# Performance work log

Hardware: AMD Instinct MI355X
Metric: run time of the kernel (lower is better)

## Reference

```python
import jax, jax.numpy as jnp
import numpy as np

NU, NBU, NI, D, L = 50000, 20000, 100000, 64, 2
C_TEMP = 0.25


def setup_inputs() -> dict:
    key = jax.random.key(0)
    ks = jax.random.split(key, 11)
    B, E_ui, E_ub, E_bi = 2048, 1_500_000, 1_000_000, 1_000_000
    return {
        "users": jax.random.randint(ks[0], (B,), 0, NU, dtype=jnp.int32),
        "bundles": jax.random.randint(ks[1], (B, 2), 0, NBU, dtype=jnp.int32),
        "ui_u": jax.random.randint(ks[2], (E_ui,), 0, NU, dtype=jnp.int32),
        "ui_i": jax.random.randint(ks[3], (E_ui,), 0, NI, dtype=jnp.int32),
        "ub_u": jax.random.randint(ks[4], (E_ub,), 0, NU, dtype=jnp.int32),
        "ub_b": jax.random.randint(ks[5], (E_ub,), 0, NBU, dtype=jnp.int32),
        "bi_b": jax.random.randint(ks[6], (E_bi,), 0, NBU, dtype=jnp.int32),
        "bi_i": jax.random.randint(ks[7], (E_bi,), 0, NI, dtype=jnp.int32),
        "users_feature": jax.random.normal(ks[8], (NU, D), jnp.float32) * 0.1,
        "bundles_feature": jax.random.normal(ks[9], (NBU, D), jnp.float32) * 0.1,
        "items_feature": jax.random.normal(ks[10], (NI, D), jnp.float32) * 0.1,
    }


def _sym_norm_vals(rows, cols, n):
    # laplace_transform: D_r^{-1/2} A D_c^{-1/2}; graph is symmetric so row/col degrees coincide
    deg = jax.ops.segment_sum(jnp.ones(rows.shape, jnp.float32), rows, num_segments=n)
    dinv = 1.0 / (jnp.sqrt(deg) + 1e-8)
    return dinv[rows] * dinv[cols]


def _spmm(rows, cols, vals, feat, n):
    return jax.ops.segment_sum(vals[:, None] * feat[cols], rows, num_segments=n)


def _one_propagate(rows, cols, n, A, Bf):
    vals = _sym_norm_vals(rows, cols, n)
    f = jnp.concatenate([A, Bf], axis=0)  # [n, D]
    acc = f
    for i in range(L):
        f = _spmm(rows, cols, vals, f, n) / (i + 2)
        nrm = jnp.maximum(jnp.linalg.norm(f, axis=1, keepdims=True), 1e-12)
        acc = acc + f / nrm  # sum of L2-normalized layer outputs + layer0
    return acc[: A.shape[0]], acc[A.shape[0]:]


def _bundle_agg(bi_b, bi_i, il_items):
    # row-normalized bundle-item aggregation: diag(1/bundle_size) @ BI
    deg = jax.ops.segment_sum(jnp.ones(bi_b.shape, jnp.float32), bi_b, num_segments=NBU)
    w = (1.0 / (deg + 1e-8))[bi_b]
    return jax.ops.segment_sum(w[:, None] * il_items[bi_i], bi_b, num_segments=NBU)


def _c_loss(pos, aug):
    pos = pos[:, 0, :]
    aug = aug[:, 0, :]
    pos = pos / jnp.maximum(jnp.linalg.norm(pos, axis=1, keepdims=True), 1e-12)
    aug = aug / jnp.maximum(jnp.linalg.norm(aug, axis=1, keepdims=True), 1e-12)
    pos_score = jnp.sum(pos * aug, axis=1) / C_TEMP
    ttl = jnp.matmul(pos, aug.T) / C_TEMP  # [B, B]
    return -jnp.mean(pos_score - jax.nn.logsumexp(ttl, axis=1))


def reference(users, bundles, ui_u, ui_i, ub_u, ub_b, bi_b, bi_i,
              users_feature, bundles_feature, items_feature):
    # item-level graph: [[0, UI], [UI^T, 0]], size NU+NI (symmetric directed edge list)
    il_rows = jnp.concatenate([ui_u, ui_i + NU])
    il_cols = jnp.concatenate([ui_i + NU, ui_u])
    IL_users, IL_items = _one_propagate(il_rows, il_cols, NU + NI, users_feature, items_feature)
    IL_bundles = _bundle_agg(bi_b, bi_i, IL_items)

    # bundle-level graph: [[0, UB], [UB^T, 0]], size NU+NBU
    bl_rows = jnp.concatenate([ub_u, ub_b + NU])
    bl_cols = jnp.concatenate([ub_b + NU, ub_u])
    BL_users, BL_bundles = _one_propagate(bl_rows, bl_cols, NU + NBU, users_feature, bundles_feature)

    nb = bundles.shape[1]
    IL_u = jnp.broadcast_to(IL_users[users][:, None, :], (users.shape[0], nb, D))
    BL_u = jnp.broadcast_to(BL_users[users][:, None, :], (users.shape[0], nb, D))
    IL_b = IL_bundles[bundles]  # [B, nb, D]
    BL_b = BL_bundles[bundles]

    pred = jnp.sum(IL_u * IL_b, axis=2) + jnp.sum(BL_u * BL_b, axis=2)  # [B, 2]
    bpr_loss = -jnp.mean(jax.nn.log_sigmoid(pred[:, 0:1] - pred[:, 1:2]))

    c_loss = 0.5 * (_c_loss(IL_u, BL_u) + _c_loss(IL_b, BL_b))
    return jnp.stack([bpr_loss, c_loss])


if __name__ == "__main__":
    out = reference(**setup_inputs())
    print(out)
```

## Files before the change

kernel.cpp:

```cpp
#include <hip/hip_runtime.h>
#include <hip/hip_bf16.h>
#include <math.h>

static constexpr int NUc  = 50000;
static constexpr int NBUc = 20000;
static constexpr int NIc  = 100000;
static constexpr int NILc = 150000;
static constexpr int NBLc = 70000;
static constexpr int GUB0   = 150016;
static constexpr int GBI0   = 220032;
static constexpr int BK_UB0 = 1172;
static constexpr int BK_BI0 = 1719;
static constexpr int NBK    = 1876;
static constexpr int GTOT   = NBK * 128;

__device__ __forceinline__ float wredsum(float v) {
  #pragma unroll
  for (int m = 32; m >= 1; m >>= 1) v += __shfl_xor(v, m, 64);
  return v;
}
__device__ __forceinline__ float bf2f(unsigned short h) {
  return __uint_as_float(((unsigned int)h) << 16);
}
__device__ __forceinline__ unsigned short f2bf(float f) {
  unsigned int u = __float_as_uint(f);
  return (unsigned short)((u + 0x7FFFu + ((u >> 16) & 1u)) >> 16);
}

__global__ void k_bcount_all(const int* __restrict__ ui_u, const int* __restrict__ ui_i,
                             const int* __restrict__ ub_u, const int* __restrict__ ub_b,
                             const int* __restrict__ bi_b,
                             int E_ui, int E_ub, int E_bi, int* __restrict__ bCnt) {
  __shared__ int hist[NBK];
  for (int i = threadIdx.x; i < NBK; i += 256) hist[i] = 0;
  __syncthreads();
  int b = blockIdx.x;
  if (b < 512) {
    int chunk = (E_ui + 511) / 512, c0 = b * chunk, c1 = min(E_ui, c0 + chunk);
    for (int e = c0 + (int)threadIdx.x; e < c1; e += 256) {
      atomicAdd(&hist[ui_u[e] >> 7], 1);
      atomicAdd(&hist[(ui_i[e] + NUc) >> 7], 1);
    }
  } else if (b < 768) {
    int lb = b - 512, chunk = (E_ub + 255) / 256, c0 = lb * chunk, c1 = min(E_ub, c0 + chunk);
    for (int e = c0 + (int)threadIdx.x; e < c1; e += 256) {
      atomicAdd(&hist[(GUB0 + ub_u[e]) >> 7], 1);
      atomicAdd(&hist[(GUB0 + NUc + ub_b[e]) >> 7], 1);
    }
  } else {
    int lb = b - 768, chunk = (E_bi + 255) / 256, c0 = lb * chunk, c1 = min(E_bi, c0 + chunk);
    for (int e = c0 + (int)threadIdx.x; e < c1; e += 256)
      atomicAdd(&hist[(GBI0 + bi_b[e]) >> 7], 1);
  }
  __syncthreads();
  for (int i = threadIdx.x; i < NBK; i += 256)
    if (hist[i]) atomicAdd(&bCnt[i], hist[i]);
}

__global__ void k_scan2048(const int* __restrict__ in, int n,
                           int* __restrict__ outBase, int* __restrict__ outCur) {
  __shared__ int sh[512];
  int t = threadIdx.x, i0 = 4 * t;
  int v0 = (i0 < n) ? in[i0] : 0;
  int v1 = (i0 + 1 < n) ? in[i0 + 1] : 0;
  int v2 = (i0 + 2 < n) ? in[i0 + 2] : 0;
  int v3 = (i0 + 3 < n) ? in[i0 + 3] : 0;
  int ts = v0 + v1 + v2 + v3;
  sh[t] = ts;
  __syncthreads();
  for (int o = 1; o < 512; o <<= 1) {
    int x = (t >= o) ? sh[t - o] : 0;
    __syncthreads();
    sh[t] += x;
    __syncthreads();
  }
  int ex = sh[t] - ts;
  if (i0 < n)     { outBase[i0] = ex;                    outCur[i0] = ex; }
  if (i0 + 1 < n) { outBase[i0 + 1] = ex + v0;           outCur[i0 + 1] = ex + v0; }
  if (i0 + 2 < n) { outBase[i0 + 2] = ex + v0 + v1;      outCur[i0 + 2] = ex + v0 + v1; }
  if (i0 + 3 < n) { outBase[i0 + 3] = ex + v0 + v1 + v2; outCur[i0 + 3] = ex + v0 + v1 + v2; }
  if (t == 511) outBase[n] = sh[511];
}

__global__ void k_bin_all(const int* __restrict__ ui_u, const int* __restrict__ ui_i,
                          const int* __restrict__ ub_u, const int* __restrict__ ub_b,
                          const int* __restrict__ bi_b, const int* __restrict__ bi_i,
                          int E_ui, int E_ub, int E_bi,
                          int* __restrict__ bCur, int2* __restrict__ binned) {
  __shared__ int hist[NBK];
  __shared__ int base[NBK];
  for (int i = threadIdx.x; i < NBK; i += 256) hist[i] = 0;
  __syncthreads();
  int b = blockIdx.x;
  int c0, c1, seg;
  if (b < 512)      { seg = 0; int ch = (E_ui + 511) / 512; c0 = b * ch; c1 = min(E_ui, c0 + ch); }
  else if (b < 768) { seg = 1; int ch = (E_ub + 255) / 256; c0 = (b - 512) * ch; c1 = min(E_ub, c0 + ch); }
  else              { seg = 2; int ch = (E_bi + 255) / 256; c0 = (b - 768) * ch; c1 = min(E_bi, c0 + ch); }
  for (int e = c0 + (int)threadIdx.x; e < c1; e += 256) {
    if (seg == 0) {
      atomicAdd(&hist[ui_u[e] >> 7], 1);
      atomicAdd(&hist[(ui_i[e] + NUc) >> 7], 1);
    } else if (seg == 1) {
      atomicAdd(&hist[(GUB0 + ub_u[e]) >> 7], 1);
      atomicAdd(&hist[(GUB0 + NUc + ub_b[e]) >> 7], 1);
    } else {
      atomicAdd(&hist[(GBI0 + bi_b[e]) >> 7], 1);
    }
  }
  __syncthreads();
  for (int i = threadIdx.x; i < NBK; i += 256) {
    int h = hist[i];
    base[i] = h ? atomicAdd(&bCur[i], h) : 0;
    hist[i] = 0;
  }
  __syncthreads();
  for (int e = c0 + (int)threadIdx.x; e < c1; e += 256) {
    if (seg == 0) {
      int u = ui_u[e], x = ui_i[e] + NUc;
      int b1 = u >> 7; binned[base[b1] + atomicAdd(&hist[b1], 1)] = make_int2(u, x);
      int b2 = x >> 7; binned[base[b2] + atomicAdd(&hist[b2], 1)] = make_int2(x, u);
    } else if (seg == 1) {
      int ul = ub_u[e], bl = NUc + ub_b[e];
      int r1 = GUB0 + ul, r2 = GUB0 + bl;
      int b1 = r1 >> 7; binned[base[b1] + atomicAdd(&hist[b1], 1)] = make_int2(r1, bl);
      int b2 = r2 >> 7; binned[base[b2] + atomicAdd(&hist[b2], 1)] = make_int2(r2, ul);
    } else {
      int r = GBI0 + bi_b[e];
      int b1 = r >> 7; binned[base[b1] + atomicAdd(&hist[b1], 1)] = make_int2(r, bi_i[e]);
    }
  }
}

__global__ void k_rowhist_all(const int2* __restrict__ binned, const int* __restrict__ bBase,
                              int* __restrict__ cnt) {
  __shared__ int hist[128];
  int bk = blockIdx.x, rowbase = bk << 7;
  int s = bBase[bk], e = bBase[bk + 1];
  if (threadIdx.x < 128) hist[threadIdx.x] = 0;
  __syncthreads();
  for (int i = s + (int)threadIdx.x; i < e; i += 256)
    atomicAdd(&hist[binned[i].x & 127], 1);
  __syncthreads();
  if (threadIdx.x < 128) cnt[rowbase + (int)threadIdx.x] = hist[threadIdx.x];
}

__global__ void k_scan_block_pad(const int* __restrict__ in, int n, int* __restrict__ out,
                                 int* __restrict__ bsum) {
  __shared__ int sh[256];
  int t = threadIdx.x;
  long base = (long)blockIdx.x * 1024 + (long)t * 4;
  int v0 = (base     < n) ? ((in[base]     + 15) & ~15) : 0;
  int v1 = (base + 1 < n) ? ((in[base + 1] + 15) & ~15) : 0;
  int v2 = (base + 2 < n) ? ((in[base + 2] + 15) & ~15) : 0;
  int v3 = (base + 3 < n) ? ((in[base + 3] + 15) & ~15) : 0;
  int tsum = v0 + v1 + v2 + v3;
  sh[t] = tsum;
  __syncthreads();
  for (int o = 1; o < 256; o <<= 1) {
    int x = (t >= o) ? sh[t - o] : 0;
    __syncthreads();
    sh[t] += x;
    __syncthreads();
  }
  int excl = sh[t] - tsum;
  if (t == 255) bsum[blockIdx.x] = sh[255];
  if (base     < n) out[base]     = excl;
  if (base + 1 < n) out[base + 1] = excl + v0;
  if (base + 2 < n) out[base + 2] = excl + v0 + v1;
  if (base + 3 < n) out[base + 3] = excl + v0 + v1 + v2;
}

__global__ void k_scan_bsum(int* __restrict__ bsum, int nb) {
  __shared__ int sh[256];
  int t = threadIdx.x;
  int v = (t < nb) ? bsum[t] : 0;
  sh[t] = v;
  __syncthreads();
  for (int o = 1; o < 256; o <<= 1) {
    int x = (t >= o) ? sh[t - o] : 0;
    __syncthreads();
    sh[t] += x;
    __syncthreads();
  }
  if (t < nb) bsum[t] = sh[t] - v;
}

__global__ void k_scan_add(int* __restrict__ out, int n, const int* __restrict__ bsum) {
  long i = (long)blockIdx.x * 256 + threadIdx.x;
  if (i < n) out[i] += bsum[i >> 10];
}

__global__ void k_csrfill_all(const int2* __restrict__ binned, const int* __restrict__ bBase,
                              const int* __restrict__ rp, int* __restrict__ colv) {
  __shared__ int cur[128];
  int bk = blockIdx.x, rowbase = bk << 7;
  int xb, zpad;
  if (bk < BK_UB0)      { xb = 0;    zpad = NILc; }
  else if (bk < BK_BI0) { xb = GUB0; zpad = GUB0 + NBLc; }
  else                  { xb = 0;    zpad = NIc; }
  int s = bBase[bk], e = bBase[bk + 1];
  if (threadIdx.x < 128) cur[threadIdx.x] = rp[rowbase + (int)threadIdx.x];
  __syncthreads();
  for (int i = s + (int)threadIdx.x; i < e; i += 256) {
    int2 rc = binned[i];
    int pos = atomicAdd(&cur[rc.x & 127], 1);
    colv[pos] = xb + rc.y;
  }
  __syncthreads();
  if (threadIdx.x < 128) {
    int r = rowbase + (int)threadIdx.x;
    int end = rp[r + 1];
    for (int k = cur[threadIdx.x]; k < end; k++) colv[k] = zpad;
  }
}

__global__ void k_prescale_all(const int* __restrict__ cnt, const float* __restrict__ userF,
                               const float* __restrict__ bundF, const float* __restrict__ itemF,
                               unsigned short* __restrict__ X) {
  long idx = (long)blockIdx.x * 256 + threadIdx.x;
  if (idx >= (long)GBI0 * 64) return;
  int g = (int)(idx >> 6), d = (int)(idx & 63);
  float v = 0.0f;
  if (g < NILc) v = (g < NUc) ? userF[(long)g * 64 + d] : itemF[(long)(g - NUc) * 64 + d];
  else if (g >= GUB0 && g < GUB0 + NBLc) {
    int l = g - GUB0;
    v = (l < NUc) ? userF[(long)l * 64 + d] : bundF[(long)(l - NUc) * 64 + d];
  }
  float dinv = 1.0f / (sqrtf((float)cnt[g]) + 1e-8f);
  X[idx] = f2bf(v * dinv);
}

__global__ void k_spmm_g(const int* __restrict__ rp, const int* __restrict__ cnt,
                         const int* __restrict__ col, const unsigned short* __restrict__ X,
                         unsigned short* __restrict__ outB, float* __restrict__ outInv,
                         float scale, int mulDinv, int n) {
  int row = blockIdx.x * 4 + (threadIdx.x >> 6);
  if (row >= n) return;
  int lane = threadIdx.x & 63, q = lane >> 4, p = lane & 15;
  int s = rp[row], e = rp[row + 1];
  const uint2* Xp = (const uint2*)X + p;
  float a0 = 0.f, a1 = 0.f, a2 = 0.f, a3 = 0.f;
  for (int eo = s + q; eo < e; eo += 16) {
    int c0 = col[eo], c1 = col[eo + 4], c2 = col[eo + 8], c3 = col[eo + 12];
    uint2 v0 = Xp[(size_t)c0 << 4];
    uint2 v1 = Xp[(size_t)c1 << 4];
    uint2 v2 = Xp[(size_t)c2 << 4];
    uint2 v3 = Xp[(size_t)c3 << 4];
    a0 += (__uint_as_float(v0.x << 16) + __uint_as_float(v1.x << 16)) +
          (__uint_as_float(v2.x << 16) + __uint_as_float(v3.x << 16));
    a1 += (__uint_as_float(v0.x & 0xFFFF0000u) + __uint_as_float(v1.x & 0xFFFF0000u)) +
          (__uint_as_float(v2.x & 0xFFFF0000u) + __uint_as_float(v3.x & 0xFFFF0000u));
    a2 += (__uint_as_float(v0.y << 16) + __uint_as_float(v1.y << 16)) +
          (__uint_as_float(v2.y << 16) + __uint_as_float(v3.y << 16));
    a3 += (__uint_as_float(v0.y & 0xFFFF0000u) + __uint_as_float(v1.y & 0xFFFF0000u)) +
          (__uint_as_float(v2.y & 0xFFFF0000u) + __uint_as_float(v3.y & 0xFFFF0000u));
  }
  a0 += __shfl_xor(a0, 32, 64); a1 += __shfl_xor(a1, 32, 64);
  a2 += __shfl_xor(a2, 32, 64); a3 += __shfl_xor(a3, 32, 64);
  a0 += __shfl_xor(a0, 16, 64); a1 += __shfl_xor(a1, 16, 64);
  a2 += __shfl_xor(a2, 16, 64); a3 += __shfl_xor(a3, 16, 64);
  float dinv = 1.0f / (sqrtf((float)cnt[row]) + 1e-8f);
  float f = dinv * scale;
  float r0 = a0 * f, r1 = a1 * f, r2 = a2 * f, r3 = a3 * f;
  float ss = r0 * r0 + r1 * r1 + r2 * r2 + r3 * r3;
  ss += __shfl_xor(ss, 8, 64); ss += __shfl_xor(ss, 4, 64);
  ss += __shfl_xor(ss, 2, 64); ss += __shfl_xor(ss, 1, 64);
  if (q == 0) {
    float mf = mulDinv ? dinv : 1.0f;
    uint2 m;
    m.x = (unsigned int)f2bf(r0 * mf) | ((unsigned int)f2bf(r1 * mf) << 16);
    m.y = (unsigned int)f2bf(r2 * mf) | ((unsigned int)f2bf(r3 * mf) << 16);
    *(uint2*)(outB + (size_t)row * 64 + p * 4) = m;
    if (p == 0) outInv[row] = 1.0f / fmaxf(sqrtf(ss), 1e-12f);
  }
}

__global__ void k_agg_g(const int* __restrict__ rp, const int* __restrict__ cnt,
                        const int* __restrict__ col, const unsigned short* __restrict__ MACC,
                        float* __restrict__ ILB, int n) {
  int rl = blockIdx.x * 4 + (threadIdx.x >> 6);
  if (rl >= n) return;
  int row = GBI0 + rl;
  int lane = threadIdx.x & 63, q = lane >> 4, p = lane & 15;
  int s = rp[row], e = rp[row + 1];
  const uint2* Xp = (const uint2*)MACC + p;
  float a0 = 0.f, a1 = 0.f, a2 = 0.f, a3 = 0.f;
  for (int eo = s + q; eo < e; eo += 16) {
    int c0 = col[eo], c1 = col[eo + 4], c2 = col[eo + 8], c3 = col[eo + 12];
    uint2 v0 = Xp[(size_t)c0 << 4];
    uint2 v1 = Xp[(size_t)c1 << 4];
    uint2 v2 = Xp[(size_t)c2 << 4];
    uint2 v3 = Xp[(size_t)c3 << 4];
    a0 += (__uint_as_float(v0.x << 16) + __uint_as_float(v1.x << 16)) +
          (__uint_as_float(v2.x << 16) + __uint_as_float(v3.x << 16));
    a1 += (__uint_as_float(v0.x & 0xFFFF0000u) + __uint_as_float(v1.x & 0xFFFF0000u)) +
          (__uint_as_float(v2.x & 0xFFFF0000u) + __uint_as_float(v3.x & 0xFFFF0000u));
    a2 += (__uint_as_float(v0.y << 16) + __uint_as_float(v1.y << 16)) +
          (__uint_as_float(v2.y << 16) + __uint_as_float(v3.y << 16));
    a3 += (__uint_as_float(v0.y & 0xFFFF0000u) + __uint_as_float(v1.y & 0xFFFF0000u)) +
          (__uint_as_float(v2.y & 0xFFFF0000u) + __uint_as_float(v3.y & 0xFFFF0000u));
  }
  a0 += __shfl_xor(a0, 32, 64); a1 += __shfl_xor(a1, 32, 64);
  a2 += __shfl_xor(a2, 32, 64); a3 += __shfl_xor(a3, 32, 64);
  a0 += __shfl_xor(a0, 16, 64); a1 += __shfl_xor(a1, 16, 64);
  a2 += __shfl_xor(a2, 16, 64); a3 += __shfl_xor(a3, 16, 64);
  if (q == 0) {
    float w = 1.0f / ((float)cnt[row] + 1e-8f);
    *(float4*)(ILB + (size_t)rl * 64 + p * 4) = make_float4(a0 * w, a1 * w, a2 * w, a3 * w);
  }
}

__global__ void k_acc_all(const float* __restrict__ userF, const float* __restrict__ bundF,
                          const float* __restrict__ itemF, const int* __restrict__ cnt,
                          const unsigned short* __restrict__ M1, const unsigned short* __restrict__ F2b,
                          const float* __restrict__ INV1, const float* __restrict__ INV2,
                          float* __restrict__ ACC, unsigned short* __restrict__ MACC) {
  long idx = (long)blockIdx.x * 256 + threadIdx.x;
  if (idx >= (long)(NILc + NBLc) * 64) return;
  int rl = (int)(idx >> 6), d = (int)(idx & 63);
  int g; float base;
  bool il = rl < NILc;
  if (il) {
    g = rl;
    base = (rl < NUc) ? userF[(long)rl * 64 + d] : itemF[(long)(rl - NUc) * 64 + d];
  } else {
    int l = rl - NILc;
    g = GUB0 + l;
    base = (l < NUc) ? userF[(long)l * 64 + d] : bundF[(long)(l - NUc) * 64 + d];
  }
  float rs = sqrtf((float)cnt[g]) + 1e-8f;
  float F1 = bf2f(M1[(size_t)g * 64 + d]) * rs;
  float F2 = bf2f(F2b[(size_t)g * 64 + d]);
  float res = base + F1 * INV1[g] + F2 * INV2[g];
  ACC[idx] = res;
  if (il && rl >= NUc) MACC[(size_t)(rl - NUc) * 64 + d] = f2bf(res);
}

__global__ void k_gather_all(const int* __restrict__ users, const int* __restrict__ bundles,
                             const float* __restrict__ ACC, const float* __restrict__ ILB, int B,
                             float* __restrict__ ILu, float* __restrict__ BLu,
                             float* __restrict__ ILb2, float* __restrict__ BLb2) {
  long i = (long)blockIdx.x * 256 + threadIdx.x;
  if (i >= (long)6 * B * 64) return;
  int r = (int)(i >> 6), d = (int)(i & 63);
  if (r < B) ILu[(long)r * 64 + d] = ACC[(long)users[r] * 64 + d];
  else if (r < 2 * B) { int rr = r - B; BLu[(long)rr * 64 + d] = ACC[(long)(NILc + users[rr]) * 64 + d]; }
  else if (r < 4 * B) { int rr = r - 2 * B; ILb2[(long)rr * 64 + d] = ILB[(long)bundles[rr] * 64 + d]; }
  else { int rr = r - 4 * B; BLb2[(long)rr * 64 + d] = ACC[(long)(NILc + NUc + bundles[rr]) * 64 + d]; }
}

__global__ void k_normalize4(const float* __restrict__ s0, const float* __restrict__ s1,
                             const float* __restrict__ s2, const float* __restrict__ s3,
                             float* __restrict__ d0, float* __restrict__ d1,
                             float* __restrict__ d2, float* __restrict__ d3, int B) {
  int row = blockIdx.x * 4 + (threadIdx.x >> 6);
  int lane = threadIdx.x & 63;
  if (row >= 4 * B) return;
  int which = row / B, r = row - which * B;
  const float* src; float* dst; int stride;
  if (which == 0)      { src = s0; dst = d0; stride = 64; }
  else if (which == 1) { src = s1; dst = d1; stride = 64; }
  else if (which == 2) { src = s2; dst = d2; stride = 128; }
  else                 { src = s3; dst = d3; stride = 128; }
  float v = src[(long)r * stride + lane];
  float ss = wredsum(v * v);
  dst[(long)r * 64 + lane] = v * (1.0f / fmaxf(sqrtf(ss), 1e-12f));
}

__global__ void k_bpr(const float* __restrict__ ILu, const float* __restrict__ ILb2,
                      const float* __restrict__ BLu, const float* __restrict__ BLb2,
                      int B, float* __restrict__ out) {
  int row = blockIdx.x * 4 + (threadIdx.x >> 6);
  int lane = threadIdx.x & 63;
  if (row >= B) return;
  float t = ILu[(long)row * 64 + lane] *
              (ILb2[(long)(2 * row) * 64 + lane] - ILb2[(long)(2 * row + 1) * 64 + lane]) +
            BLu[(long)row * 64 + lane] *
              (BLb2[(long)(2 * row) * 64 + lane] - BLb2[(long)(2 * row + 1) * 64 + lane]);
  float x = wredsum(t);
  if (lane == 0) {
    float ls = -(fmaxf(-x, 0.0f) + log1pf(expf(-fabsf(x))));
    unsafeAtomicAdd(&out[0], -ls / (float)B);
  }
}

__global__ void k_gemm_nt2(const float* __restrict__ P1, const float* __restrict__ A1,
                           const float* __restrict__ P2, const float* __restrict__ A2,
                           float* __restrict__ S1o, float* __restrict__ S2o,
                           int N, float scale) {
  __shared__ float Ps[64][129];
  __shared__ float As[64][129];
  const float* P = blockIdx.z ? P2 : P1;
  const float* A = blockIdx.z ? A2 : A1;
  float* S = blockIdx.z ? S2o : S1o;
  int bi0 = blockIdx.y * 128, bj0 = blockIdx.x * 128;
  int t = threadIdx.x;
  #pragma unroll
  for (int sct = 0; sct < 8; sct++) {
    int idx4 = t + sct * 256;
    int r = idx4 >> 4, k = (idx4 & 15) << 2;
    int pr = min(bi0 + r, N - 1);
    int ar = min(bj0 + r, N - 1);
    float4 v = *(const float4*)(P + (long)pr * 64 + k);
    Ps[k][r] = v.x; Ps[k + 1][r] = v.y; Ps[k + 2][r] = v.z; Ps[k + 3][r] = v.w;
    float4 w = *(const float4*)(A + (long)ar * 64 + k);
    As[k][r] = w.x; As[k + 1][r] = w.y; As[k + 2][r] = w.z; As[k + 3][r] = w.w;
  }
  __syncthreads();
  int tx = t & 15, ty = t >> 4;
  float acc[8][8];
  #pragma unroll
  for (int i = 0; i < 8; i++)
    #pragma unroll
    for (int j = 0; j < 8; j++) acc[i][j] = 0.0f;
  #pragma unroll 4
  for (int k = 0; k < 64; k++) {
    float a[8], b[8];
    #pragma unroll
    for (int i = 0; i < 8; i++) a[i] = Ps[k][ty * 8 + i];
    #pragma unroll
    for (int j = 0; j < 8; j++) b[j] = As[k][tx + 16 * j];
    #pragma unroll
    for (int i = 0; i < 8; i++)
      #pragma unroll
      for (int j = 0; j < 8; j++) acc[i][j] = fmaf(a[i], b[j], acc[i][j]);
  }
  #pragma unroll
  for (int i = 0; i < 8; i++) {
    int row = bi0 + ty * 8 + i;
    if (row >= N) continue;
    #pragma unroll
    for (int j = 0; j < 8; j++) {
      int cc = bj0 + tx + 16 * j;
      if (cc < N) S[(long)row * N + cc] = acc[i][j] * scale;
    }
  }
}

__global__ void k_lse2(const float* __restrict__ S1, const float* __restrict__ S2,
                       int B, float coeff, float* __restrict__ out) {
  constexpr float L2E = 1.44269504f;
  int row = blockIdx.x * 4 + (threadIdx.x >> 6);
  int lane = threadIdx.x & 63;
  const float* Sr; int dg;
  if (row < B) { Sr = S1 + (long)row * B; dg = row; }
  else         { Sr = S2 + (long)(row - B) * B; dg = row - B; }
  float m = -1e30f, s = 0.0f;
  for (int w = 0; w < (B >> 8); w++) {
    float4 v = *(const float4*)(Sr + ((w << 6) + lane) * 4);
    float mx = fmaxf(fmaxf(v.x, v.y), fmaxf(v.z, v.w));
    if (mx > m) { s *= exp2f((m - mx) * L2E); m = mx; }
    s += exp2f((v.x - m) * L2E) + exp2f((v.y - m) * L2E) +
         exp2f((v.z - m) * L2E) + exp2f((v.w - m) * L2E);
  }
  #pragma unroll
  for (int o = 32; o >= 1; o >>= 1) {
    float m2 = __shfl_xor(m, o, 64), s2 = __shfl_xor(s, o, 64);
    float M = fmaxf(m, m2);
    s = s * exp2f((m - M) * L2E) + s2 * exp2f((m2 - M) * L2E);
    m = M;
  }
  if (lane == 0) {
    float lse = m + log2f(s) * 0.69314718f;
    unsafeAtomicAdd(&out[1], -(Sr[dg] - lse) * coeff);
  }
}

extern "C" void kernel_launch(void* const* d_in, const int* in_sizes, int n_in,
                              void* d_out, int out_size, void* d_ws, size_t ws_size,
                              hipStream_t stream) {
  const int* users   = (const int*)d_in[0];
  const int* bundles = (const int*)d_in[1];
  const int* ui_u    = (const int*)d_in[2];
  const int* ui_i    = (const int*)d_in[3];
  const int* ub_u    = (const int*)d_in[4];
  const int* ub_b    = (const int*)d_in[5];
  const int* bi_b    = (const int*)d_in[6];
  const int* bi_i    = (const int*)d_in[7];
  const float* userF = (const float*)d_in[8];
  const float* bundF = (const float*)d_in[9];
  const float* itemF = (const float*)d_in[10];
  float* out = (float*)d_out;

  const int B    = in_sizes[0];
  const int E_ui = in_sizes[2];
  const int E_ub = in_sizes[4];
  const int E_bi = in_sizes[6];
  const long E_all = 2L * E_ui + 2L * E_ub + E_bi;

  float* ws = (float*)d_ws;
  size_t off = 0;
  auto alloc = [&](size_t nfloat) -> float* {
    float* p = ws + off;
    off += (nfloat + 63) & ~(size_t)63;
    return p;
  };
  float* ACC = alloc((size_t)(NILc + NBLc) * 64);
  unsigned short* X  = (unsigned short*)alloc((size_t)GBI0 * 32);
  unsigned short* M1 = (unsigned short*)alloc((size_t)GBI0 * 32);
  int2* binned = (int2*)alloc((size_t)E_all * 2);
  int* colv  = (int*)alloc((size_t)E_all + 15 * (size_t)GTOT + 128);
  int* rp    = (int*)alloc(GTOT + 1);
  int* cnt   = (int*)alloc(GTOT + 1);
  float* INV1 = alloc(GTOT);
  float* INV2 = alloc(GTOT);
  float* ILB  = alloc((size_t)NBUc * 64);
  float* ILu  = alloc((size_t)B * 64);
  float* BLu  = alloc((size_t)B * 64);
  float* ILb2 = alloc((size_t)B * 128);
  float* BLb2 = alloc((size_t)B * 128);
  float* PN1  = alloc((size_t)B * 64);
  float* AN1  = alloc((size_t)B * 64);
  float* PN2  = alloc((size_t)B * 64);
  float* AN2  = alloc((size_t)B * 64);
  int* bCnt  = (int*)alloc(2049);
  int* bBase = (int*)alloc(2049);
  int* bCur  = (int*)alloc(2049);
  int* bsum  = (int*)alloc(256);
  (void)ws_size; (void)n_in; (void)out_size;

  unsigned short* F2b  = X;
  unsigned short* MACC = (unsigned short*)binned;
  float* S1 = ACC;
  float* S2 = ACC + (size_t)B * B;

  hipMemsetAsync(bCnt, 0, sizeof(int) * NBK, stream);
  k_bcount_all<<<1024, 256, 0, stream>>>(ui_u, ui_i, ub_u, ub_b, bi_b, E_ui, E_ub, E_bi, bCnt);
  k_scan2048<<<1, 512, 0, stream>>>(bCnt, NBK, bBase, bCur);
  k_bin_all<<<1024, 256, 0, stream>>>(ui_u, ui_i, ub_u, ub_b, bi_b, bi_i,
                                      E_ui, E_ub, E_bi, bCur, binned);
  hipMemsetAsync(cnt, 0, sizeof(int) * (GTOT + 1), stream);
  k_rowhist_all<<<NBK, 256, 0, stream>>>(binned, bBase, cnt);
  {
    int scan_n = GTOT + 1;
    int nb1 = (scan_n + 1023) / 1024;
    k_scan_block_pad<<<nb1, 256, 0, stream>>>(cnt, scan_n, rp, bsum);
    k_scan_bsum<<<1, 256, 0, stream>>>(bsum, nb1);
    k_scan_add<<<(scan_n + 255) / 256, 256, 0, stream>>>(rp, scan_n, bsum);
  }
  k_csrfill_all<<<NBK, 256, 0, stream>>>(binned, bBase, rp, colv);

  k_prescale_all<<<(int)(((long)GBI0 * 64 + 255) / 256), 256, 0, stream>>>(cnt, userF, bundF,
                                                                           itemF, X);
  k_spmm_g<<<(GBI0 + 3) / 4, 256, 0, stream>>>(rp, cnt, colv, X, M1, INV1, 0.5f, 1, GBI0);
  k_spmm_g<<<(GBI0 + 3) / 4, 256, 0, stream>>>(rp, cnt, colv, M1, F2b, INV2, 1.0f / 3.0f, 0, GBI0);
  hipMemsetAsync(MACC + (size_t)NIc * 64, 0, 128, stream);
  k_acc_all<<<(int)(((long)(NILc + NBLc) * 64 + 255) / 256), 256, 0, stream>>>(
      userF, bundF, itemF, cnt, M1, F2b, INV1, INV2, ACC, MACC);
  k_agg_g<<<(NBUc + 3) / 4, 256, 0, stream>>>(rp, cnt, colv, MACC, ILB, NBUc);
  k_gather_all<<<(int)(((long)6 * B * 64 + 255) / 256), 256, 0, stream>>>(
      users, bundles, ACC, ILB, B, ILu, BLu, ILb2, BLb2);

  hipMemsetAsync(out, 0, 2 * sizeof(float), stream);
  k_bpr<<<(B + 3) / 4, 256, 0, stream>>>(ILu, ILb2, BLu, BLb2, B, out);
  k_normalize4<<<(4 * B + 3) / 4, 256, 0, stream>>>(ILu, BLu, ILb2, BLb2, PN1, AN1, PN2, AN2, B);
  dim3 gg((B + 127) / 128, (B + 127) / 128, 2);
  k_gemm_nt2<<<gg, 256, 0, stream>>>(PN1, AN1, PN2, AN2, S1, S2, B, 4.0f);
  k_lse2<<<(2 * B + 3) / 4, 256, 0, stream>>>(S1, S2, B, 0.5f / (float)B, out);
}
```

Baseline: 575.7 us.

## Pack binned edges into 32 bits and compute accumulations only for batch rows

Edge records in the binning stage are packed into one 32-bit word: the row's low 7 bits sit in the top bits and the column in the low 18 bits. This halves the scatter and read traffic of the intermediate edge buffer. The full-size ACC accumulation over all user, bundle and item rows is replaced by an items-only pass feeding bundle aggregation, plus a per-batch kernel that computes user and bundle accumulations on demand. That kernel also does the L2 normalization, removing the separate gather and normalize kernels and the large ACC buffer. The similarity matrices now reuse the X and M1 buffers, which relies on column indices staying below 2^18 and on those buffers being dead by the GEMM.

```diff
diff --git a/kernel.cpp b/kernel.cpp
--- a/kernel.cpp
+++ b/kernel.cpp
@@ -86,7 +86,7 @@
                           const int* __restrict__ ub_u, const int* __restrict__ ub_b,
                           const int* __restrict__ bi_b, const int* __restrict__ bi_i,
                           int E_ui, int E_ub, int E_bi,
-                          int* __restrict__ bCur, int2* __restrict__ binned) {
+                          int* __restrict__ bCur, unsigned int* __restrict__ binned) {
   __shared__ int hist[NBK];
   __shared__ int base[NBK];
   for (int i = threadIdx.x; i < NBK; i += 256) hist[i] = 0;
@@ -117,21 +117,26 @@
   for (int e = c0 + (int)threadIdx.x; e < c1; e += 256) {
     if (seg == 0) {
       int u = ui_u[e], x = ui_i[e] + NUc;
-      int b1 = u >> 7; binned[base[b1] + atomicAdd(&hist[b1], 1)] = make_int2(u, x);
-      int b2 = x >> 7; binned[base[b2] + atomicAdd(&hist[b2], 1)] = make_int2(x, u);
+      int b1 = u >> 7;
+      binned[base[b1] + atomicAdd(&hist[b1], 1)] = ((unsigned)(u & 127) << 18) | (unsigned)x;
+      int b2 = x >> 7;
+      binned[base[b2] + atomicAdd(&hist[b2], 1)] = ((unsigned)(x & 127) << 18) | (unsigned)u;
     } else if (seg == 1) {
       int ul = ub_u[e], bl = NUc + ub_b[e];
       int r1 = GUB0 + ul, r2 = GUB0 + bl;
-      int b1 = r1 >> 7; binned[base[b1] + atomicAdd(&hist[b1], 1)] = make_int2(r1, bl);
-      int b2 = r2 >> 7; binned[base[b2] + atomicAdd(&hist[b2], 1)] = make_int2(r2, ul);
+      int b1 = r1 >> 7;
+      binned[base[b1] + atomicAdd(&hist[b1], 1)] = ((unsigned)(r1 & 127) << 18) | (unsigned)bl;
+      int b2 = r2 >> 7;
+      binned[base[b2] + atomicAdd(&hist[b2], 1)] = ((unsigned)(r2 & 127) << 18) | (unsigned)ul;
     } else {
       int r = GBI0 + bi_b[e];
-      int b1 = r >> 7; binned[base[b1] + atomicAdd(&hist[b1], 1)] = make_int2(r, bi_i[e]);
+      int b1 = r >> 7;
+      binned[base[b1] + atomicAdd(&hist[b1], 1)] = ((unsigned)(r & 127) << 18) | (unsigned)bi_i[e];
     }
   }
 }
 
-__global__ void k_rowhist_all(const int2* __restrict__ binned, const int* __restrict__ bBase,
+__global__ void k_rowhist_all(const unsigned int* __restrict__ binned, const int* __restrict__ bBase,
                               int* __restrict__ cnt) {
   __shared__ int hist[128];
   int bk = blockIdx.x, rowbase = bk << 7;
@@ -139,7 +144,7 @@
   if (threadIdx.x < 128) hist[threadIdx.x] = 0;
   __syncthreads();
   for (int i = s + (int)threadIdx.x; i < e; i += 256)
-    atomicAdd(&hist[binned[i].x & 127], 1);
+    atomicAdd(&hist[binned[i] >> 18], 1);
   __syncthreads();
   if (threadIdx.x < 128) cnt[rowbase + (int)threadIdx.x] = hist[threadIdx.x];
 }
@@ -190,7 +195,7 @@
   if (i < n) out[i] += bsum[i >> 10];
 }
 
-__global__ void k_csrfill_all(const int2* __restrict__ binned, const int* __restrict__ bBase,
+__global__ void k_csrfill_all(const unsigned int* __restrict__ binned, const int* __restrict__ bBase,
                               const int* __restrict__ rp, int* __restrict__ colv) {
   __shared__ int cur[128];
   int bk = blockIdx.x, rowbase = bk << 7;
@@ -202,9 +207,9 @@
   if (threadIdx.x < 128) cur[threadIdx.x] = rp[rowbase + (int)threadIdx.x];
   __syncthreads();
   for (int i = s + (int)threadIdx.x; i < e; i += 256) {
-    int2 rc = binned[i];
-    int pos = atomicAdd(&cur[rc.x & 127], 1);
-    colv[pos] = xb + rc.y;
+    unsigned int pk = binned[i];
+    int pos = atomicAdd(&cur[pk >> 18], 1);
+    colv[pos] = xb + (int)(pk & 0x3FFFFu);
   }
   __syncthreads();
   if (threadIdx.x < 128) {
@@ -310,61 +315,64 @@
   }
 }
 
-__global__ void k_acc_all(const float* __restrict__ userF, const float* __restrict__ bundF,
-                          const float* __restrict__ itemF, const int* __restrict__ cnt,
-                          const unsigned short* __restrict__ M1, const unsigned short* __restrict__ F2b,
-                          const float* __restrict__ INV1, const float* __restrict__ INV2,
-                          float* __restrict__ ACC, unsigned short* __restrict__ MACC) {
+__global__ void k_acc_items(const float* __restrict__ itemF, const int* __restrict__ cnt,
+                            const unsigned short* __restrict__ M1, const unsigned short* __restrict__ F2b,
+                            const float* __restrict__ INV1, const float* __restrict__ INV2,
+                            unsigned short* __restrict__ MACC) {
   long idx = (long)blockIdx.x * 256 + threadIdx.x;
-  if (idx >= (long)(NILc + NBLc) * 64) return;
-  int rl = (int)(idx >> 6), d = (int)(idx & 63);
-  int g; float base;
-  bool il = rl < NILc;
-  if (il) {
-    g = rl;
-    base = (rl < NUc) ? userF[(long)rl * 64 + d] : itemF[(long)(rl - NUc) * 64 + d];
+  if (idx >= (long)NIc * 64) return;
+  int rl = (int)(idx >> 6);
+  int g = NUc + rl;
+  long gi = (long)g * 64 + (idx & 63);
+  float rs = sqrtf((float)cnt[g]) + 1e-8f;
+  float res = itemF[idx] + bf2f(M1[gi]) * rs * INV1[g] + bf2f(F2b[gi]) * INV2[g];
+  MACC[idx] = f2bf(res);
+}
+
+__global__ void k_batch(const int* __restrict__ users, const int* __restrict__ bundles,
+                        const float* __restrict__ userF, const float* __restrict__ bundF,
+                        const int* __restrict__ cnt,
+                        const unsigned short* __restrict__ M1, const unsigned short* __restrict__ F2b,
+                        const float* __restrict__ INV1, const float* __restrict__ INV2,
+                        const float* __restrict__ ILB, int B,
+                        float* __restrict__ ILu, float* __restrict__ BLu,
+                        float* __restrict__ ILb2, float* __restrict__ BLb2,
+                        float* __restrict__ PN1, float* __restrict__ AN1,
+                        float* __restrict__ PN2, float* __restrict__ AN2) {
+  int w = blockIdx.x * 4 + (threadIdx.x >> 6);
+  int lane = threadIdx.x & 63;
+  if (w >= 6 * B) return;
+  float val;
+  float* rawDst; float* nrmDst = nullptr; int nrmRow = 0;
+  if (w < 2 * B) {
+    bool il = w < B;
+    int j = il ? w : w - B;
+    int u = users[j];
+    int g = il ? u : GUB0 + u;
+    long gi = (long)g * 64 + lane;
+    float rs = sqrtf((float)cnt[g]) + 1e-8f;
+    val = userF[(long)u * 64 + lane] + bf2f(M1[gi]) * rs * INV1[g] + bf2f(F2b[gi]) * INV2[g];
+    rawDst = (il ? ILu : BLu) + (long)j * 64;
+    nrmDst = il ? PN1 : AN1; nrmRow = j;
+  } else if (w < 4 * B) {
+    int j = w - 2 * B;
+    int b = bundles[j];
+    val = ILB[(long)b * 64 + lane];
+    rawDst = ILb2 + (long)j * 64;
+    if ((j & 1) == 0) { nrmDst = PN2; nrmRow = j >> 1; }
   } else {
-    int l = rl - NILc;
-    g = GUB0 + l;
-    base = (l < NUc) ? userF[(long)l * 64 + d] : bundF[(long)(l - NUc) * 64 + d];
-  }
-  float rs = sqrtf((float)cnt[g]) + 1e-8f;
-  float F1 = bf2f(M1[(size_t)g * 64 + d]) * rs;
-  float F2 = bf2f(F2b[(size_t)g * 64 + d]);
-  float res = base + F1 * INV1[g] + F2 * INV2[g];
-  ACC[idx] = res;
-  if (il && rl >= NUc) MACC[(size_t)(rl - NUc) * 64 + d] = f2bf(res);
-}
-
-__global__ void k_gather_all(const int* __restrict__ users, const int* __restrict__ bundles,
-                             const float* __restrict__ ACC, const float* __restrict__ ILB, int B,
-                             float* __restrict__ ILu, float* __restrict__ BLu,
-                             float* __restrict__ ILb2, float* __restrict__ BLb2) {
-  long i = (long)blockIdx.x * 256 + threadIdx.x;
-  if (i >= (long)6 * B * 64) return;
-  int r = (int)(i >> 6), d = (int)(i & 63);
-  if (r < B) ILu[(long)r * 64 + d] = ACC[(long)users[r] * 64 + d];
-  else if (r < 2 * B) { int rr = r - B; BLu[(long)rr * 64 + d] = ACC[(long)(NILc + users[rr]) * 64 + d]; }
-  else if (r < 4 * B) { int rr = r - 2 * B; ILb2[(long)rr * 64 + d] = ILB[(long)bundles[rr] * 64 + d]; }
-  else { int rr = r - 4 * B; BLb2[(long)rr * 64 + d] = ACC[(long)(NILc + NUc + bundles[rr]) * 64 + d]; }
-}
-
-__global__ void k_normalize4(const float* __restrict__ s0, const float* __restrict__ s1,
-                             const float* __restrict__ s2, const float* __restrict__ s3,
-                             float* __restrict__ d0, float* __restrict__ d1,
-                             float* __restrict__ d2, float* __restrict__ d3, int B) {
-  int row = blockIdx.x * 4 + (threadIdx.x >> 6);
-  int lane = threadIdx.x & 63;
-  if (row >= 4 * B) return;
-  int which = row / B, r = row - which * B;
-  const float* src; float* dst; int stride;
-  if (which == 0)      { src = s0; dst = d0; stride = 64; }
-  else if (which == 1) { src = s1; dst = d1; stride = 64; }
-  else if (which == 2) { src = s2; dst = d2; stride = 128; }
-  else                 { src = s3; dst = d3; stride = 128; }
-  float v = src[(long)r * stride + lane];
-  float ss = wredsum(v * v);
-  dst[(long)r * 64 + lane] = v * (1.0f / fmaxf(sqrtf(ss), 1e-12f));
+    int j = w - 4 * B;
+    int b = bundles[j];
+    int g = GUB0 + NUc + b;
+    long gi = (long)g * 64 + lane;
+    float rs = sqrtf((float)cnt[g]) + 1e-8f;
+    val = bundF[(long)b * 64 + lane] + bf2f(M1[gi]) * rs * INV1[g] + bf2f(F2b[gi]) * INV2[g];
+    rawDst = BLb2 + (long)j * 64;
+    if ((j & 1) == 0) { nrmDst = AN2; nrmRow = j >> 1; }
+  }
+  rawDst[lane] = val;
+  float ss = wredsum(val * val);
+  if (nrmDst) nrmDst[(long)nrmRow * 64 + lane] = val * (1.0f / fmaxf(sqrtf(ss), 1e-12f));
 }
 
 __global__ void k_bpr(const float* __restrict__ ILu, const float* __restrict__ ILb2,
@@ -495,10 +503,9 @@
     off += (nfloat + 63) & ~(size_t)63;
     return p;
   };
-  float* ACC = alloc((size_t)(NILc + NBLc) * 64);
   unsigned short* X  = (unsigned short*)alloc((size_t)GBI0 * 32);
   unsigned short* M1 = (unsigned short*)alloc((size_t)GBI0 * 32);
-  int2* binned = (int2*)alloc((size_t)E_all * 2);
+  unsigned int* binned = (unsigned int*)alloc((size_t)E_all);
   int* colv  = (int*)alloc((size_t)E_all + 15 * (size_t)GTOT + 128);
   int* rp    = (int*)alloc(GTOT + 1);
   int* cnt   = (int*)alloc(GTOT + 1);
@@ -521,8 +528,8 @@
 
   unsigned short* F2b  = X;
   unsigned short* MACC = (unsigned short*)binned;
-  float* S1 = ACC;
-  float* S2 = ACC + (size_t)B * B;
+  float* S1 = (float*)X;
+  float* S2 = (float*)M1;
 
   hipMemsetAsync(bCnt, 0, sizeof(int) * NBK, stream);
   k_bcount_all<<<1024, 256, 0, stream>>>(ui_u, ui_i, ub_u, ub_b, bi_b, E_ui, E_ub, E_bi, bCnt);
@@ -545,15 +552,15 @@
   k_spmm_g<<<(GBI0 + 3) / 4, 256, 0, stream>>>(rp, cnt, colv, X, M1, INV1, 0.5f, 1, GBI0);
   k_spmm_g<<<(GBI0 + 3) / 4, 256, 0, stream>>>(rp, cnt, colv, M1, F2b, INV2, 1.0f / 3.0f, 0, GBI0);
   hipMemsetAsync(MACC + (size_t)NIc * 64, 0, 128, stream);
-  k_acc_all<<<(int)(((long)(NILc + NBLc) * 64 + 255) / 256), 256, 0, stream>>>(
-      userF, bundF, itemF, cnt, M1, F2b, INV1, INV2, ACC, MACC);
+  k_acc_items<<<(int)(((long)NIc * 64 + 255) / 256), 256, 0, stream>>>(
+      itemF, cnt, M1, F2b, INV1, INV2, MACC);
   k_agg_g<<<(NBUc + 3) / 4, 256, 0, stream>>>(rp, cnt, colv, MACC, ILB, NBUc);
-  k_gather_all<<<(int)(((long)6 * B * 64 + 255) / 256), 256, 0, stream>>>(
-      users, bundles, ACC, ILB, B, ILu, BLu, ILb2, BLb2);
+  k_batch<<<(6 * B + 3) / 4, 256, 0, stream>>>(users, bundles, userF, bundF, cnt, M1, F2b,
+                                               INV1, INV2, ILB, B,
+                                               ILu, BLu, ILb2, BLb2, PN1, AN1, PN2, AN2);
 
   hipMemsetAsync(out, 0, 2 * sizeof(float), stream);
   k_bpr<<<(B + 3) / 4, 256, 0, stream>>>(ILu, ILb2, BLu, BLb2, B, out);
-  k_normalize4<<<(4 * B + 3) / 4, 256, 0, stream>>>(ILu, BLu, ILb2, BLb2, PN1, AN1, PN2, AN2, B);
   dim3 gg((B + 127) / 128, (B + 127) / 128, 2);
   k_gemm_nt2<<<gg, 256, 0, stream>>>(PN1, AN1, PN2, AN2, S1, S2, B, 4.0f);
   k_lse2<<<(2 * B + 3) / 4, 256, 0, stream>>>(S1, S2, B, 0.5f / (float)B, out);
```

After: 531.7 us. 7.6% less time.
